# Kernel tuning notes

Hardware: AMD Instinct MI355X
Metric: run time of the kernel (lower is better)

## Reference

```python
import jax, jax.numpy as jnp
import numpy as np

N = 100_000   # nodes
E = 1_600_000 # edges per graph
D = 64        # feature width
HA = 32       # attention hidden


def setup_inputs() -> dict:
    key = jax.random.key(0)
    ks = jax.random.split(key, 20)
    inp = {}
    inp["h"] = jax.random.normal(ks[0], (N, D), jnp.float32)
    inp["e_od"] = jax.random.normal(ks[1], (E, D), jnp.float32)
    inp["e_ad"] = jax.random.normal(ks[2], (E, D), jnp.float32)
    inp["src_od"] = jax.random.randint(ks[3], (E,), 0, N)
    inp["dst_od"] = jax.random.randint(ks[4], (E,), 0, N)
    inp["src_ad"] = jax.random.randint(ks[5], (E,), 0, N)
    inp["dst_ad"] = jax.random.randint(ks[6], (E,), 0, N)
    s = 1.0 / np.sqrt(D).astype(np.float32)
    # stacked params: index 0 = OD graph, index 1 = AD graph
    inp["W_src"]  = jax.random.normal(ks[7],  (2, D, D), jnp.float32) * s
    inp["W_dst"]  = jax.random.normal(ks[8],  (2, D, D), jnp.float32) * s
    inp["W_edge"] = jax.random.normal(ks[9],  (2, D, D), jnp.float32) * s
    inp["b_msg"]  = jnp.zeros((2, D), jnp.float32)
    inp["W_self"] = jax.random.normal(ks[10], (2, D, D), jnp.float32) * s
    inp["W_agg"]  = jax.random.normal(ks[11], (2, D, D), jnp.float32) * s
    inp["b_node"] = jnp.zeros((2, D), jnp.float32)
    # Attention (Aggregate_samedim): Linear(D->HA, bias) -> tanh -> Linear(HA->1, no bias)
    inp["attn_l1_w"] = jax.random.normal(ks[12], (D, HA), jnp.float32) * s
    inp["attn_l1_b"] = jnp.zeros((HA,), jnp.float32)
    inp["attn_l2_w"] = jax.random.normal(ks[13], (HA, 1), jnp.float32) * (1.0 / np.sqrt(HA).astype(np.float32))
    return inp


def reference(h, e_od, e_ad, src_od, dst_od, src_ad, dst_ad,
              W_src, W_dst, W_edge, b_msg, W_self, W_agg, b_node,
              attn_l1_w, attn_l1_b, attn_l2_w):
    def mpnn(i, e, src, dst):
        # edge message: gather src/dst node feats, small GEMMs, relu  [E, D]
        m = jax.nn.relu(h[src] @ W_src[i] + h[dst] @ W_dst[i] + e @ W_edge[i] + b_msg[i])
        # scatter-sum to destination nodes  [N, D]
        agg = jax.ops.segment_sum(m, dst, num_segments=N)
        # node update  [N, D]
        return jax.nn.relu(h @ W_self[i] + agg @ W_agg[i] + b_node[i])

    intra = mpnn(0, e_od, src_od, dst_od)  # OD graph node states
    inter = mpnn(1, e_ad, src_ad, dst_ad)  # AD graph node states
    # Aggregate_samedim: attention over the 2-way stack
    rep = jnp.stack([intra, inter], axis=1)               # [N, 2, D]
    w = jnp.tanh(rep @ attn_l1_w + attn_l1_b) @ attn_l2_w  # [N, 2, 1]
    beta = jax.nn.softmax(w, axis=1)
    return (beta * rep).sum(axis=1)                        # [N, D]
```

## Files before the change

### kernel.cpp

```cpp
#include <hip/hip_runtime.h>
#include <hip/hip_bf16.h>

using short8  = __attribute__((ext_vector_type(8))) short;
using ushort8 = __attribute__((ext_vector_type(8))) unsigned short;
using f32x4   = __attribute__((ext_vector_type(4))) float;
using fvec4   = __attribute__((ext_vector_type(4))) float;

#define CH 8192

__device__ inline unsigned short f2bf(float x) {
  union { __hip_bfloat16 b; unsigned short u; } c;
  c.b = __float2bfloat16(x);
  return c.u;
}
__device__ inline float bf2f(unsigned short s) {
  return __uint_as_float(((unsigned int)s) << 16);
}
__device__ inline unsigned int pk2(float lo, float hi) {
  union { __hip_bfloat162 b; unsigned int u; } c;
  c.b = __float22bfloat162_rn(make_float2(lo, hi));
  return c.u;
}
__device__ inline short8 cvt8(fvec4 a, fvec4 b) {
  union { short8 s; unsigned int u[4]; } r;
  r.u[0] = pk2(a[0], a[1]);
  r.u[1] = pk2(a[2], a[3]);
  r.u[2] = pk2(b[0], b[1]);
  r.u[3] = pk2(b[2], b[3]);
  return r.s;
}

__device__ inline void load_bfrags_f32(const float* __restrict__ W, short8 bfr[2][4], int lane) {
  int l15 = lane & 15, lh = lane >> 4;
#pragma unroll
  for (int ks = 0; ks < 2; ++ks)
#pragma unroll
    for (int ct = 0; ct < 4; ++ct) {
      short8 v;
#pragma unroll
      for (int i = 0; i < 8; ++i)
        v[i] = (short)f2bf(W[(ks * 32 + lh * 8 + i) * 64 + ct * 16 + l15]);
      bfr[ks][ct] = v;
    }
}

__device__ inline void load_bfrags(const unsigned short* __restrict__ Wf, short8 bfr[2][4], int lane) {
#pragma unroll
  for (int ks = 0; ks < 2; ++ks)
#pragma unroll
    for (int ct = 0; ct < 4; ++ct) {
      union { ushort8 u; short8 s; } c;
      c.u = *reinterpret_cast<const ushort8*>(Wf + (((ks * 4 + ct) << 9) + (lane << 3)));
      bfr[ks][ct] = c.s;
    }
}

struct PrepArgs {
  const float* W[10];
};

__global__ __launch_bounds__(64) void prep_w_kernel(PrepArgs pw, unsigned short* __restrict__ Wf) {
  int z = blockIdx.x;
  int lane = threadIdx.x & 63;
  short8 bfr[2][4];
  load_bfrags_f32(pw.W[z], bfr, lane);
  unsigned short* dst = Wf + (size_t)z * 4096;
#pragma unroll
  for (int ks = 0; ks < 2; ++ks)
#pragma unroll
    for (int ct = 0; ct < 4; ++ct) {
      union { short8 s; ushort8 u; } c;
      c.s = bfr[ks][ct];
      *reinterpret_cast<ushort8*>(dst + (((ks * 4 + ct) << 9) + (lane << 3))) = c.u;
    }
}

struct ProjArgs {
  unsigned short* out[6];
};

__global__ __launch_bounds__(256) void proj_all_kernel(const float* __restrict__ h,
                                                       const unsigned short* __restrict__ Wf,
                                                       ProjArgs pa, int N) {
  int lane = threadIdx.x & 63;
  int wv = threadIdx.x >> 6;
  int rowbase = blockIdx.x * 256 + wv * 64;
  int l15 = lane & 15, lh = lane >> 4;

  short8 afr[4][2];
#pragma unroll
  for (int rt = 0; rt < 4; ++rt) {
    int row = rowbase + rt * 16 + l15;
    int rc = row < N ? row : 0;
    const fvec4* p = reinterpret_cast<const fvec4*>(h + (size_t)rc * 64);
#pragma unroll
    for (int ks = 0; ks < 2; ++ks)
      afr[rt][ks] = cvt8(p[ks * 8 + lh * 2], p[ks * 8 + lh * 2 + 1]);
  }

  for (int z = 0; z < 6; ++z) {
    short8 bfr[2][4];
    load_bfrags(Wf + (size_t)z * 4096, bfr, lane);
    unsigned short* __restrict__ out = pa.out[z];

    f32x4 acc[4][4];
#pragma unroll
    for (int rt = 0; rt < 4; ++rt)
#pragma unroll
      for (int ct = 0; ct < 4; ++ct) acc[rt][ct] = (f32x4){0.f, 0.f, 0.f, 0.f};

#pragma unroll
    for (int rt = 0; rt < 4; ++rt)
#pragma unroll
      for (int ks = 0; ks < 2; ++ks)
#pragma unroll
        for (int ct = 0; ct < 4; ++ct)
          acc[rt][ct] = __builtin_amdgcn_mfma_f32_16x16x32_bf16(afr[rt][ks], bfr[ks][ct], acc[rt][ct], 0, 0, 0);

#pragma unroll
    for (int rt = 0; rt < 4; ++rt)
#pragma unroll
      for (int rg = 0; rg < 4; ++rg) {
        int row = rowbase + rt * 16 + lh * 4 + rg;
        if (row < N) {
#pragma unroll
          for (int ct = 0; ct < 4; ++ct)
            out[(size_t)row * 64 + ct * 16 + l15] = f2bf(acc[rt][ct][rg]);
        }
      }
  }
}

__global__ __launch_bounds__(256) void hist_kernel(const int* __restrict__ dst0, const int* __restrict__ dst1,
                                                   int* __restrict__ counts, int E, int NBK) {
  __shared__ int hcnt[2048];
  int z = blockIdx.y;
  const int* __restrict__ dst = z ? dst1 : dst0;
  int t = threadIdx.x;
  for (int i = t; i < NBK; i += 256) hcnt[i] = 0;
  __syncthreads();
  int base = blockIdx.x * CH;
#pragma unroll 4
  for (int k = 0; k < CH / 256; ++k) {
    int i = base + k * 256 + t;
    if (i < E) atomicAdd(&hcnt[dst[i] >> 6], 1);
  }
  __syncthreads();
  for (int i = t; i < NBK; i += 256) {
    int c = hcnt[i];
    if (c) atomicAdd(&counts[(size_t)z * NBK + i], c);
  }
}

__global__ __launch_bounds__(1024) void scan_kernel(const int* __restrict__ counts, int* __restrict__ cursor,
                                                    int* __restrict__ gcur, int NBK) {
  int z = blockIdx.x;
  const int* c = counts + (size_t)z * NBK;
  __shared__ int lds[1024];
  int t = threadIdx.x;
  int carry = 0;
  for (int base = 0; base < NBK; base += 1024) {
    int i = base + t;
    int v = (i < NBK) ? c[i] : 0;
    lds[t] = v;
    __syncthreads();
    for (int off = 1; off < 1024; off <<= 1) {
      int x = (t >= off) ? lds[t - off] : 0;
      __syncthreads();
      lds[t] += x;
      __syncthreads();
    }
    if (i < NBK) {
      int excl = carry + lds[t] - v;
      cursor[(size_t)z * NBK + i] = excl;
      gcur[(size_t)z * NBK + i] = excl;
    }
    carry += lds[1023];
    __syncthreads();
  }
}

__global__ __launch_bounds__(256) void scatterA_kernel(
    const int* __restrict__ src0, const int* __restrict__ dst0,
    const int* __restrict__ src1, const int* __restrict__ dst1,
    int* __restrict__ gcur, int2* __restrict__ recs0, int2* __restrict__ recs1,
    int E, int NBK) {
  __shared__ int lcnt[2048];
  int z = blockIdx.y;
  const int* __restrict__ src = z ? src1 : src0;
  const int* __restrict__ dst = z ? dst1 : dst0;
  int2* __restrict__ recs = z ? recs1 : recs0;
  int t = threadIdx.x;
  for (int i = t; i < NBK; i += 256) lcnt[i] = 0;
  __syncthreads();
  int base = blockIdx.x * CH;
#pragma unroll 4
  for (int k = 0; k < CH / 256; ++k) {
    int i = base + k * 256 + t;
    if (i < E) atomicAdd(&lcnt[dst[i] >> 6], 1);
  }
  __syncthreads();
  for (int i = t; i < NBK; i += 256) {
    int c = lcnt[i];
    lcnt[i] = c ? atomicAdd(&gcur[(size_t)z * NBK + i], c) : 0;
  }
  __syncthreads();
#pragma unroll 4
  for (int k = 0; k < CH / 256; ++k) {
    int i = base + k * 256 + t;
    if (i < E) {
      int d = dst[i], s = src[i];
      int bin = d >> 6, dl = d & 63;
      int pos = atomicAdd(&lcnt[bin], 1);
      recs[pos] = make_int2(i | (bin << 21), s | (dl << 26));
    }
  }
}

__global__ __launch_bounds__(256) void sortB_kernel(int2* __restrict__ recs0, int2* __restrict__ recs1,
                                                    const int* __restrict__ cursor,
                                                    const int* __restrict__ counts, int NBK) {
  __shared__ int cnt_lds[64];
  __shared__ int cur_lds[64];
  int z = blockIdx.y;
  int b = blockIdx.x;
  int2* __restrict__ recs = z ? recs1 : recs0;
  int start = cursor[(size_t)z * NBK + b];
  int cnt = counts[(size_t)z * NBK + b];
  int t = threadIdx.x;

  for (int cbase = 0; cbase < cnt; cbase += 2048) {
    int ccnt = min(2048, cnt - cbase);
    int2 r[8];
    int dl[8];
    if (t < 64) cnt_lds[t] = 0;
    __syncthreads();
#pragma unroll
    for (int k = 0; k < 8; ++k) {
      int idx = k * 256 + t;
      if (idx < ccnt) {
        r[k] = recs[start + cbase + idx];
        dl[k] = ((unsigned)r[k].y) >> 26;
        atomicAdd(&cnt_lds[dl[k]], 1);
      }
    }
    __syncthreads();
    if (t < 64) {
      int c = cnt_lds[t];
      int x = c;
#pragma unroll
      for (int off = 1; off < 64; off <<= 1) {
        int y = __shfl_up(x, off);
        if (t >= off) x += y;
      }
      cur_lds[t] = x - c;
    }
    __syncthreads();
#pragma unroll
    for (int k = 0; k < 8; ++k) {
      int idx = k * 256 + t;
      if (idx < ccnt) {
        int pos = atomicAdd(&cur_lds[dl[k]], 1);
        recs[start + cbase + pos] = r[k];
      }
    }
    __syncthreads();
  }
}

struct EdgeArgs {
  const float* e[2];
  const int2* recs[2];
  const unsigned short* We[2];
  const float* bmsg[2];
  const unsigned short* Ps[2];
  const unsigned short* Pd[2];
  float* agg[2];
};

__global__ __launch_bounds__(256) void edge_sorted_kernel(EdgeArgs ea, int E) {
  int z = blockIdx.y;
  const float* __restrict__ e = ea.e[z];
  const int2* __restrict__ recs = ea.recs[z];
  const unsigned short* __restrict__ Psrc = ea.Ps[z];
  const unsigned short* __restrict__ Pdst = ea.Pd[z];
  float* __restrict__ agg = ea.agg[z];

  int lane = threadIdx.x & 63;
  int wv = threadIdx.x >> 6;
  int base = (blockIdx.x * 4 + wv) * 64;
  if (base >= E) return;
  int l15 = lane & 15, lh = lane >> 4;

  int slot = base + lane;
  int el = 0, sl = 0, dl = 0;
  if (slot < E) {
    int2 rc = recs[slot];
    el = rc.x & 0x1FFFFF;
    sl = rc.y & 0x3FFFFFF;
    dl = (((rc.x >> 21) & 0x7FF) << 6) | (int)(((unsigned)rc.y) >> 26);
  }

  short8 bfr[2][4];
  load_bfrags(ea.We[z], bfr, lane);

  short8 idf[2];
#pragma unroll
  for (int half = 0; half < 2; ++half) {
    short8 v;
#pragma unroll
    for (int i = 0; i < 8; ++i)
      v[i] = (short)((lh * 8 + i == half * 16 + l15) ? 0x3F80 : 0);
    idf[half] = v;
  }

  const float* bmsg = ea.bmsg[z];
  f32x4 acc[4][4];
#pragma unroll
  for (int ct = 0; ct < 4; ++ct) {
    float b = bmsg[ct * 16 + l15];
    f32x4 bb = (f32x4){b, b, b, b};
#pragma unroll
    for (int rt = 0; rt < 4; ++rt) acc[rt][ct] = bb;
  }

#pragma unroll
  for (int rt = 0; rt < 4; ++rt) {
    int sr = rt * 16 + l15;
    int er = __shfl(el, sr);
    int hr = __shfl(sl, sr);
    int dr = __shfl(dl, sr);
    const fvec4* pr = reinterpret_cast<const fvec4*>(e + ((size_t)er << 6));
    const ushort8* ps = reinterpret_cast<const ushort8*>(Psrc + ((size_t)hr << 6));
    const ushort8* pd = reinterpret_cast<const ushort8*>(Pdst + ((size_t)dr << 6));
    short8 aE0 = cvt8(pr[lh * 2], pr[lh * 2 + 1]);
    short8 aE1 = cvt8(pr[8 + lh * 2], pr[8 + lh * 2 + 1]);
    union { ushort8 u; short8 s; } aP0, aP1, aD0, aD1;
    aP0.u = ps[lh];
    aP1.u = ps[4 + lh];
    aD0.u = pd[lh];
    aD1.u = pd[4 + lh];
#pragma unroll
    for (int ct = 0; ct < 4; ++ct) {
      acc[rt][ct] = __builtin_amdgcn_mfma_f32_16x16x32_bf16(aE0, bfr[0][ct], acc[rt][ct], 0, 0, 0);
      acc[rt][ct] = __builtin_amdgcn_mfma_f32_16x16x32_bf16(aE1, bfr[1][ct], acc[rt][ct], 0, 0, 0);
    }
    acc[rt][0] = __builtin_amdgcn_mfma_f32_16x16x32_bf16(aP0.s, idf[0], acc[rt][0], 0, 0, 0);
    acc[rt][1] = __builtin_amdgcn_mfma_f32_16x16x32_bf16(aP0.s, idf[1], acc[rt][1], 0, 0, 0);
    acc[rt][2] = __builtin_amdgcn_mfma_f32_16x16x32_bf16(aP1.s, idf[0], acc[rt][2], 0, 0, 0);
    acc[rt][3] = __builtin_amdgcn_mfma_f32_16x16x32_bf16(aP1.s, idf[1], acc[rt][3], 0, 0, 0);
    acc[rt][0] = __builtin_amdgcn_mfma_f32_16x16x32_bf16(aD0.s, idf[0], acc[rt][0], 0, 0, 0);
    acc[rt][1] = __builtin_amdgcn_mfma_f32_16x16x32_bf16(aD0.s, idf[1], acc[rt][1], 0, 0, 0);
    acc[rt][2] = __builtin_amdgcn_mfma_f32_16x16x32_bf16(aD1.s, idf[0], acc[rt][2], 0, 0, 0);
    acc[rt][3] = __builtin_amdgcn_mfma_f32_16x16x32_bf16(aD1.s, idf[1], acc[rt][3], 0, 0, 0);
  }

#pragma unroll
  for (int rt = 0; rt < 4; ++rt)
#pragma unroll
    for (int ct = 0; ct < 4; ++ct)
#pragma unroll
      for (int rg = 0; rg < 4; ++rg)
        acc[rt][ct][rg] = fmaxf(acc[rt][ct][rg], 0.f);

  int dprev = __shfl_up(dl, 1);
  unsigned long long bnd = __ballot(lane > 0 && dl != dprev);
  int vrows = min(64, E - base);

  int r0 = 0;
  while (r0 < vrows) {
    unsigned long long rest = (r0 < 63) ? (bnd >> (r0 + 1)) : 0ull;
    int r1 = rest ? (r0 + 1 + __builtin_ctzll(rest)) : 64;
    if (r1 > vrows) r1 = vrows;
    int dcur = __shfl(dl, r0);

    float s0 = 0.f, s1 = 0.f, s2 = 0.f, s3 = 0.f;
#pragma unroll
    for (int rt = 0; rt < 4; ++rt) {
      int rs = rt * 16;
      if (r0 <= rs && r1 >= rs + 16) {
#pragma unroll
        for (int rg = 0; rg < 4; ++rg) {
          s0 += acc[rt][0][rg];
          s1 += acc[rt][1][rg];
          s2 += acc[rt][2][rg];
          s3 += acc[rt][3][rg];
        }
      } else if (r0 < rs + 16 && r1 > rs) {
#pragma unroll
        for (int rg = 0; rg < 4; ++rg) {
          int row = rs + lh * 4 + rg;
          bool in = (row >= r0) && (row < r1);
          s0 += in ? acc[rt][0][rg] : 0.f;
          s1 += in ? acc[rt][1][rg] : 0.f;
          s2 += in ? acc[rt][2][rg] : 0.f;
          s3 += in ? acc[rt][3][rg] : 0.f;
        }
      }
    }
    s0 += __shfl_xor(s0, 16); s0 += __shfl_xor(s0, 32);
    s1 += __shfl_xor(s1, 16); s1 += __shfl_xor(s1, 32);
    s2 += __shfl_xor(s2, 16); s2 += __shfl_xor(s2, 32);
    s3 += __shfl_xor(s3, 16); s3 += __shfl_xor(s3, 32);
    float mine = (lh == 0) ? s0 : (lh == 1) ? s1 : (lh == 2) ? s2 : s3;
    atomicAdd(&agg[(size_t)dcur * 64 + lane], mine);
    r0 = r1;
  }
}

struct NodeArgs {
  const float* agg[2];
  const unsigned short* T[2];
  const float* bn[2];
  unsigned short* U[2];
};

__global__ __launch_bounds__(256) void node_kernel(const unsigned short* __restrict__ Wf,
                                                   NodeArgs na, int N) {
  int z = blockIdx.y;
  const float* __restrict__ agg = na.agg[z];
  const unsigned short* __restrict__ T = na.T[z];
  const float* __restrict__ bn = na.bn[z];
  unsigned short* __restrict__ U = na.U[z];
  int lane = threadIdx.x & 63;
  int wv = threadIdx.x >> 6;
  int rowbase = blockIdx.x * 256 + wv * 64;
  int l15 = lane & 15, lh = lane >> 4;

  short8 bfr[2][4];
  load_bfrags(Wf + (size_t)(8 + z) * 4096, bfr, lane);

  f32x4 acc[4][4];
#pragma unroll
  for (int rt = 0; rt < 4; ++rt)
#pragma unroll
    for (int ct = 0; ct < 4; ++ct) acc[rt][ct] = (f32x4){0.f, 0.f, 0.f, 0.f};

#pragma unroll
  for (int rt = 0; rt < 4; ++rt) {
    int row = rowbase + rt * 16 + l15;
    int rc = row < N ? row : 0;
    const fvec4* p = reinterpret_cast<const fvec4*>(agg + (size_t)rc * 64);
#pragma unroll
    for (int ks = 0; ks < 2; ++ks) {
      fvec4 p0 = p[ks * 8 + lh * 2], p1 = p[ks * 8 + lh * 2 + 1];
      short8 ahi = cvt8(p0, p1);
      fvec4 q0, q1;
#pragma unroll
      for (int i = 0; i < 4; ++i) {
        q0[i] = p0[i] - bf2f((unsigned short)ahi[i]);
        q1[i] = p1[i] - bf2f((unsigned short)ahi[i + 4]);
      }
      short8 alo = cvt8(q0, q1);
#pragma unroll
      for (int ct = 0; ct < 4; ++ct) {
        acc[rt][ct] = __builtin_amdgcn_mfma_f32_16x16x32_bf16(ahi, bfr[ks][ct], acc[rt][ct], 0, 0, 0);
        acc[rt][ct] = __builtin_amdgcn_mfma_f32_16x16x32_bf16(alo, bfr[ks][ct], acc[rt][ct], 0, 0, 0);
      }
    }
  }

  float bv[4];
#pragma unroll
  for (int ct = 0; ct < 4; ++ct) bv[ct] = bn[ct * 16 + l15];

#pragma unroll
  for (int rt = 0; rt < 4; ++rt)
#pragma unroll
    for (int rg = 0; rg < 4; ++rg) {
      int row = rowbase + rt * 16 + lh * 4 + rg;
      if (row < N) {
#pragma unroll
        for (int ct = 0; ct < 4; ++ct) {
          int c = ct * 16 + l15;
          float v = acc[rt][ct][rg] + bf2f(T[(size_t)row * 64 + c]) + bv[ct];
          U[(size_t)row * 64 + c] = f2bf(fmaxf(v, 0.0f));
        }
      }
    }
}

__global__ __launch_bounds__(256) void attn_kernel(
    const unsigned short* __restrict__ U0, const unsigned short* __restrict__ U1,
    const float* __restrict__ l1w, const float* __restrict__ l1b, const float* __restrict__ l2w,
    float* __restrict__ out, int N) {
  int t = threadIdx.x;
  int node = blockIdx.x * 64 + (t >> 2);
  int q = t & 3;
  if (node >= N) return;
  size_t b0 = (size_t)node * 64;

  float a0[8], a1[8];
#pragma unroll
  for (int i = 0; i < 8; ++i) { a0[i] = l1b[q * 8 + i]; a1[i] = a0[i]; }

  for (int k = 0; k < 64; ++k) {
    float u0 = bf2f(U0[b0 + k]);
    float u1 = bf2f(U1[b0 + k]);
#pragma unroll
    for (int i = 0; i < 8; ++i) {
      float w = l1w[k * 32 + q * 8 + i];
      a0[i] += u0 * w;
      a1[i] += u1 * w;
    }
  }
  float w0 = 0.f, w1 = 0.f;
#pragma unroll
  for (int i = 0; i < 8; ++i) {
    float l2 = l2w[q * 8 + i];
    w0 += tanhf(a0[i]) * l2;
    w1 += tanhf(a1[i]) * l2;
  }
  w0 += __shfl_xor(w0, 1, 4); w0 += __shfl_xor(w0, 2, 4);
  w1 += __shfl_xor(w1, 1, 4); w1 += __shfl_xor(w1, 2, 4);

  float m = fmaxf(w0, w1);
  float e0 = expf(w0 - m), e1 = expf(w1 - m);
  float inv = 1.0f / (e0 + e1);
  float be0 = e0 * inv, be1 = e1 * inv;

#pragma unroll
  for (int j = 0; j < 16; ++j) {
    int c = q * 16 + j;
    out[b0 + c] = be0 * bf2f(U0[b0 + c]) + be1 * bf2f(U1[b0 + c]);
  }
}

static inline size_t au(size_t x) { return (x + 255) & ~(size_t)255; }

extern "C" void kernel_launch(void* const* d_in, const int* in_sizes, int n_in,
                              void* d_out, int out_size, void* d_ws, size_t ws_size,
                              hipStream_t stream) {
  const float* h      = (const float*)d_in[0];
  const float* e_od   = (const float*)d_in[1];
  const float* e_ad   = (const float*)d_in[2];
  const int* src_od   = (const int*)d_in[3];
  const int* dst_od   = (const int*)d_in[4];
  const int* src_ad   = (const int*)d_in[5];
  const int* dst_ad   = (const int*)d_in[6];
  const float* W_src  = (const float*)d_in[7];
  const float* W_dst  = (const float*)d_in[8];
  const float* W_edge = (const float*)d_in[9];
  const float* b_msg  = (const float*)d_in[10];
  const float* W_self = (const float*)d_in[11];
  const float* W_agg  = (const float*)d_in[12];
  const float* b_node = (const float*)d_in[13];
  const float* l1w    = (const float*)d_in[14];
  const float* l1b    = (const float*)d_in[15];
  const float* l2w    = (const float*)d_in[16];
  float* out = (float*)d_out;

  int N = in_sizes[0] / 64;
  int E = in_sizes[1] / 64;
  int NBK = (N + 63) >> 6;

  char* ws = (char*)d_ws;
  size_t off = 0;
  int* counts = (int*)(ws + off);   off += au((size_t)2 * NBK * sizeof(int));
  float* agg0 = (float*)(ws + off); off += (size_t)N * 64 * sizeof(float);
  float* agg1 = (float*)(ws + off); off += (size_t)N * 64 * sizeof(float);
  size_t zero_bytes = off;
  int* cursor = (int*)(ws + off);   off += au((size_t)2 * NBK * sizeof(int));
  int* gcur   = (int*)(ws + off);   off += au((size_t)2 * NBK * sizeof(int));
  int2* recs0 = (int2*)(ws + off);  off += au((size_t)E * sizeof(int2));
  int2* recs1 = (int2*)(ws + off);  off += au((size_t)E * sizeof(int2));
  unsigned short* Wf = (unsigned short*)(ws + off); off += au((size_t)10 * 4096 * sizeof(unsigned short));
  size_t NP = au((size_t)N * 64 * sizeof(unsigned short));
  unsigned short* Psrc0 = (unsigned short*)(ws + off); off += NP;
  unsigned short* Pdst0 = (unsigned short*)(ws + off); off += NP;
  unsigned short* Psrc1 = (unsigned short*)(ws + off); off += NP;
  unsigned short* Pdst1 = (unsigned short*)(ws + off); off += NP;
  unsigned short* T0    = (unsigned short*)(ws + off); off += NP;
  unsigned short* T1    = (unsigned short*)(ws + off); off += NP;
  unsigned short* U0 = Psrc0;
  unsigned short* U1 = Psrc1;

  hipMemsetAsync(ws, 0, zero_bytes, stream);

  PrepArgs pw;
  pw.W[0] = W_src;         pw.W[1] = W_dst;
  pw.W[2] = W_src + 4096;  pw.W[3] = W_dst + 4096;
  pw.W[4] = W_self;        pw.W[5] = W_self + 4096;
  pw.W[6] = W_edge;        pw.W[7] = W_edge + 4096;
  pw.W[8] = W_agg;         pw.W[9] = W_agg + 4096;
  prep_w_kernel<<<10, 64, 0, stream>>>(pw, Wf);

  int nb = (N + 255) / 256;
  ProjArgs pa;
  pa.out[0] = Psrc0;
  pa.out[1] = Pdst0;
  pa.out[2] = Psrc1;
  pa.out[3] = Pdst1;
  pa.out[4] = T0;
  pa.out[5] = T1;
  proj_all_kernel<<<nb, 256, 0, stream>>>(h, Wf, pa, N);

  int nch = (E + CH - 1) / CH;
  hist_kernel<<<dim3(nch, 2), 256, 0, stream>>>(dst_od, dst_ad, counts, E, NBK);
  scan_kernel<<<2, 1024, 0, stream>>>(counts, cursor, gcur, NBK);
  scatterA_kernel<<<dim3(nch, 2), 256, 0, stream>>>(src_od, dst_od, src_ad, dst_ad, gcur,
                                                    recs0, recs1, E, NBK);
  sortB_kernel<<<dim3(NBK, 2), 256, 0, stream>>>(recs0, recs1, cursor, counts, NBK);

  int tiles = (E + 63) / 64;
  int eb = (tiles + 3) / 4;
  EdgeArgs ea;
  ea.e[0] = e_od;  ea.recs[0] = recs0; ea.We[0] = Wf + 6 * 4096; ea.bmsg[0] = b_msg;
  ea.Ps[0] = Psrc0; ea.Pd[0] = Pdst0; ea.agg[0] = agg0;
  ea.e[1] = e_ad;  ea.recs[1] = recs1; ea.We[1] = Wf + 7 * 4096; ea.bmsg[1] = b_msg + 64;
  ea.Ps[1] = Psrc1; ea.Pd[1] = Pdst1; ea.agg[1] = agg1;
  edge_sorted_kernel<<<dim3(eb, 2), 256, 0, stream>>>(ea, E);

  NodeArgs na;
  na.agg[0] = agg0; na.T[0] = T0; na.bn[0] = b_node;      na.U[0] = U0;
  na.agg[1] = agg1; na.T[1] = T1; na.bn[1] = b_node + 64; na.U[1] = U1;
  node_kernel<<<dim3(nb, 2), 256, 0, stream>>>(Wf, na, N);

  attn_kernel<<<(N + 63) / 64, 256, 0, stream>>>(U0, U1, l1w, l1b, l2w, out, N);
}
```

Baseline: 587.8 us.

## Stage edge gathers through LDS with direct global-to-LDS loads, smaller edge tiles

The edge kernel now handles 16 edges per wave instead of 64. It gathers edge features and projected src/dst rows straight into swizzled LDS with global_load_lds, then reads MFMA fragments from LDS. The goal is to raise memory-level parallelism and occupancy on the gather-bound edge stage, at the cost of four times as many waves and more redundant weight-fragment loads per edge. The projection kernel is also split across a 3-wide grid so each block computes 2 of the 6 projections, trading repeated reads of h for more parallel blocks.

```diff
diff --git a/kernel.cpp b/kernel.cpp
--- a/kernel.cpp
+++ b/kernel.cpp
@@ -30,6 +30,12 @@
   return r.s;
 }
 
+__device__ inline void gload_lds16(const void* g, void* l) {
+  __builtin_amdgcn_global_load_lds(
+      (const __attribute__((address_space(1))) void*)g,
+      (__attribute__((address_space(3))) void*)l, 16, 0, 0);
+}
+
 __device__ inline void load_bfrags_f32(const float* __restrict__ W, short8 bfr[2][4], int lane) {
   int l15 = lane & 15, lh = lane >> 4;
 #pragma unroll
@@ -82,6 +88,7 @@
 __global__ __launch_bounds__(256) void proj_all_kernel(const float* __restrict__ h,
                                                        const unsigned short* __restrict__ Wf,
                                                        ProjArgs pa, int N) {
+  int zb = blockIdx.y * 2;
   int lane = threadIdx.x & 63;
   int wv = threadIdx.x >> 6;
   int rowbase = blockIdx.x * 256 + wv * 64;
@@ -98,7 +105,8 @@
       afr[rt][ks] = cvt8(p[ks * 8 + lh * 2], p[ks * 8 + lh * 2 + 1]);
   }
 
-  for (int z = 0; z < 6; ++z) {
+  for (int zi = 0; zi < 2; ++zi) {
+    int z = zb + zi;
     short8 bfr[2][4];
     load_bfrags(Wf + (size_t)z * 4096, bfr, lane);
     unsigned short* __restrict__ out = pa.out[z];
@@ -279,6 +287,8 @@
 };
 
 __global__ __launch_bounds__(256) void edge_sorted_kernel(EdgeArgs ea, int E) {
+  __shared__ char lds_all[4][8192];
+
   int z = blockIdx.y;
   const float* __restrict__ e = ea.e[z];
   const int2* __restrict__ recs = ea.recs[z];
@@ -288,11 +298,12 @@
 
   int lane = threadIdx.x & 63;
   int wv = threadIdx.x >> 6;
-  int base = (blockIdx.x * 4 + wv) * 64;
+  int base = (blockIdx.x * 4 + wv) * 16;
   if (base >= E) return;
   int l15 = lane & 15, lh = lane >> 4;
-
-  int slot = base + lane;
+  char* lb = &lds_all[wv][0];
+
+  int slot = base + l15;
   int el = 0, sl = 0, dl = 0;
   if (slot < E) {
     int2 rc = recs[slot];
@@ -301,6 +312,34 @@
     dl = (((rc.x >> 21) & 0x7FF) << 6) | (int)(((unsigned)rc.y) >> 26);
   }
 
+#pragma unroll
+  for (int i = 0; i < 4; ++i) {
+    int r = i * 4 + (lane >> 4);
+    int er = __shfl(el, r);
+    int c = (lane & 15) ^ (r & 7);
+    gload_lds16(e + ((size_t)er << 6) + c * 4, lb + i * 1024);
+  }
+#pragma unroll
+  for (int i = 0; i < 2; ++i) {
+    int r = i * 8 + (lane >> 3);
+    int hr = __shfl(sl, r);
+    int c = (lane & 7) ^ (r & 7);
+    gload_lds16(Psrc + ((size_t)hr << 6) + c * 8, lb + 4096 + i * 1024);
+  }
+#pragma unroll
+  for (int i = 0; i < 2; ++i) {
+    int r = i * 8 + (lane >> 3);
+    int dr = __shfl(dl, r);
+    int c = (lane & 7) ^ (r & 7);
+    gload_lds16(Pdst + ((size_t)dr << 6) + c * 8, lb + 6144 + i * 1024);
+  }
+  __builtin_amdgcn_sched_barrier(0);
+
+  const float* bmsg = ea.bmsg[z];
+  float bv[4];
+#pragma unroll
+  for (int ct = 0; ct < 4; ++ct) bv[ct] = bmsg[ct * 16 + l15];
+
   short8 bfr[2][4];
   load_bfrags(ea.We[z], bfr, lane);
 
@@ -314,88 +353,81 @@
     idf[half] = v;
   }
 
-  const float* bmsg = ea.bmsg[z];
-  f32x4 acc[4][4];
-#pragma unroll
-  for (int ct = 0; ct < 4; ++ct) {
-    float b = bmsg[ct * 16 + l15];
-    f32x4 bb = (f32x4){b, b, b, b};
-#pragma unroll
-    for (int rt = 0; rt < 4; ++rt) acc[rt][ct] = bb;
-  }
-
-#pragma unroll
-  for (int rt = 0; rt < 4; ++rt) {
-    int sr = rt * 16 + l15;
-    int er = __shfl(el, sr);
-    int hr = __shfl(sl, sr);
-    int dr = __shfl(dl, sr);
-    const fvec4* pr = reinterpret_cast<const fvec4*>(e + ((size_t)er << 6));
-    const ushort8* ps = reinterpret_cast<const ushort8*>(Psrc + ((size_t)hr << 6));
-    const ushort8* pd = reinterpret_cast<const ushort8*>(Pdst + ((size_t)dr << 6));
-    short8 aE0 = cvt8(pr[lh * 2], pr[lh * 2 + 1]);
-    short8 aE1 = cvt8(pr[8 + lh * 2], pr[8 + lh * 2 + 1]);
-    union { ushort8 u; short8 s; } aP0, aP1, aD0, aD1;
-    aP0.u = ps[lh];
-    aP1.u = ps[4 + lh];
-    aD0.u = pd[lh];
-    aD1.u = pd[4 + lh];
+  f32x4 acc[4];
+#pragma unroll
+  for (int ct = 0; ct < 4; ++ct)
+    acc[ct] = (f32x4){bv[ct], bv[ct], bv[ct], bv[ct]};
+
+  asm volatile("s_waitcnt vmcnt(0)" ::: "memory");
+  __builtin_amdgcn_sched_barrier(0);
+
+  int r = l15;
+  int xs = r & 7;
+
+  union { ushort8 u; short8 s; } aP0, aP1, aD0, aD1;
+  aP0.u = *reinterpret_cast<ushort8*>(lb + 4096 + (r << 7) + (((lh) ^ xs) << 4));
+  aP1.u = *reinterpret_cast<ushort8*>(lb + 4096 + (r << 7) + (((4 + lh) ^ xs) << 4));
+  aD0.u = *reinterpret_cast<ushort8*>(lb + 6144 + (r << 7) + (((lh) ^ xs) << 4));
+  aD1.u = *reinterpret_cast<ushort8*>(lb + 6144 + (r << 7) + (((4 + lh) ^ xs) << 4));
+  acc[0] = __builtin_amdgcn_mfma_f32_16x16x32_bf16(aP0.s, idf[0], acc[0], 0, 0, 0);
+  acc[1] = __builtin_amdgcn_mfma_f32_16x16x32_bf16(aP0.s, idf[1], acc[1], 0, 0, 0);
+  acc[2] = __builtin_amdgcn_mfma_f32_16x16x32_bf16(aP1.s, idf[0], acc[2], 0, 0, 0);
+  acc[3] = __builtin_amdgcn_mfma_f32_16x16x32_bf16(aP1.s, idf[1], acc[3], 0, 0, 0);
+  acc[0] = __builtin_amdgcn_mfma_f32_16x16x32_bf16(aD0.s, idf[0], acc[0], 0, 0, 0);
+  acc[1] = __builtin_amdgcn_mfma_f32_16x16x32_bf16(aD0.s, idf[1], acc[1], 0, 0, 0);
+  acc[2] = __builtin_amdgcn_mfma_f32_16x16x32_bf16(aD1.s, idf[0], acc[2], 0, 0, 0);
+  acc[3] = __builtin_amdgcn_mfma_f32_16x16x32_bf16(aD1.s, idf[1], acc[3], 0, 0, 0);
+
+  {
+    int rb = r << 8;
+    fvec4 p0 = *reinterpret_cast<const fvec4*>(lb + rb + (((lh * 2) ^ xs) << 4));
+    fvec4 p1 = *reinterpret_cast<const fvec4*>(lb + rb + (((lh * 2 + 1) ^ xs) << 4));
+    fvec4 p2 = *reinterpret_cast<const fvec4*>(lb + rb + (((8 + lh * 2) ^ xs) << 4));
+    fvec4 p3 = *reinterpret_cast<const fvec4*>(lb + rb + (((9 + lh * 2) ^ xs) << 4));
+    short8 aE0 = cvt8(p0, p1);
+    short8 aE1 = cvt8(p2, p3);
 #pragma unroll
     for (int ct = 0; ct < 4; ++ct) {
-      acc[rt][ct] = __builtin_amdgcn_mfma_f32_16x16x32_bf16(aE0, bfr[0][ct], acc[rt][ct], 0, 0, 0);
-      acc[rt][ct] = __builtin_amdgcn_mfma_f32_16x16x32_bf16(aE1, bfr[1][ct], acc[rt][ct], 0, 0, 0);
-    }
-    acc[rt][0] = __builtin_amdgcn_mfma_f32_16x16x32_bf16(aP0.s, idf[0], acc[rt][0], 0, 0, 0);
-    acc[rt][1] = __builtin_amdgcn_mfma_f32_16x16x32_bf16(aP0.s, idf[1], acc[rt][1], 0, 0, 0);
-    acc[rt][2] = __builtin_amdgcn_mfma_f32_16x16x32_bf16(aP1.s, idf[0], acc[rt][2], 0, 0, 0);
-    acc[rt][3] = __builtin_amdgcn_mfma_f32_16x16x32_bf16(aP1.s, idf[1], acc[rt][3], 0, 0, 0);
-    acc[rt][0] = __builtin_amdgcn_mfma_f32_16x16x32_bf16(aD0.s, idf[0], acc[rt][0], 0, 0, 0);
-    acc[rt][1] = __builtin_amdgcn_mfma_f32_16x16x32_bf16(aD0.s, idf[1], acc[rt][1], 0, 0, 0);
-    acc[rt][2] = __builtin_amdgcn_mfma_f32_16x16x32_bf16(aD1.s, idf[0], acc[rt][2], 0, 0, 0);
-    acc[rt][3] = __builtin_amdgcn_mfma_f32_16x16x32_bf16(aD1.s, idf[1], acc[rt][3], 0, 0, 0);
-  }
-
-#pragma unroll
-  for (int rt = 0; rt < 4; ++rt)
-#pragma unroll
-    for (int ct = 0; ct < 4; ++ct)
-#pragma unroll
-      for (int rg = 0; rg < 4; ++rg)
-        acc[rt][ct][rg] = fmaxf(acc[rt][ct][rg], 0.f);
+      acc[ct] = __builtin_amdgcn_mfma_f32_16x16x32_bf16(aE0, bfr[0][ct], acc[ct], 0, 0, 0);
+      acc[ct] = __builtin_amdgcn_mfma_f32_16x16x32_bf16(aE1, bfr[1][ct], acc[ct], 0, 0, 0);
+    }
+  }
+
+#pragma unroll
+  for (int ct = 0; ct < 4; ++ct)
+#pragma unroll
+    for (int rg = 0; rg < 4; ++rg)
+      acc[ct][rg] = fmaxf(acc[ct][rg], 0.f);
 
   int dprev = __shfl_up(dl, 1);
-  unsigned long long bnd = __ballot(lane > 0 && dl != dprev);
-  int vrows = min(64, E - base);
+  unsigned long long bnd = __ballot(lane > 0 && dl != dprev) & 0xFFFFull;
+  int vrows = min(16, E - base);
 
   int r0 = 0;
   while (r0 < vrows) {
-    unsigned long long rest = (r0 < 63) ? (bnd >> (r0 + 1)) : 0ull;
-    int r1 = rest ? (r0 + 1 + __builtin_ctzll(rest)) : 64;
+    unsigned long long rest = bnd >> (r0 + 1);
+    int r1 = rest ? (r0 + 1 + __builtin_ctzll(rest)) : 16;
     if (r1 > vrows) r1 = vrows;
     int dcur = __shfl(dl, r0);
 
     float s0 = 0.f, s1 = 0.f, s2 = 0.f, s3 = 0.f;
-#pragma unroll
-    for (int rt = 0; rt < 4; ++rt) {
-      int rs = rt * 16;
-      if (r0 <= rs && r1 >= rs + 16) {
-#pragma unroll
-        for (int rg = 0; rg < 4; ++rg) {
-          s0 += acc[rt][0][rg];
-          s1 += acc[rt][1][rg];
-          s2 += acc[rt][2][rg];
-          s3 += acc[rt][3][rg];
-        }
-      } else if (r0 < rs + 16 && r1 > rs) {
-#pragma unroll
-        for (int rg = 0; rg < 4; ++rg) {
-          int row = rs + lh * 4 + rg;
-          bool in = (row >= r0) && (row < r1);
-          s0 += in ? acc[rt][0][rg] : 0.f;
-          s1 += in ? acc[rt][1][rg] : 0.f;
-          s2 += in ? acc[rt][2][rg] : 0.f;
-          s3 += in ? acc[rt][3][rg] : 0.f;
-        }
+    if (r0 == 0 && r1 == 16) {
+#pragma unroll
+      for (int rg = 0; rg < 4; ++rg) {
+        s0 += acc[0][rg];
+        s1 += acc[1][rg];
+        s2 += acc[2][rg];
+        s3 += acc[3][rg];
+      }
+    } else {
+#pragma unroll
+      for (int rg = 0; rg < 4; ++rg) {
+        int row = lh * 4 + rg;
+        bool in = (row >= r0) && (row < r1);
+        s0 += in ? acc[0][rg] : 0.f;
+        s1 += in ? acc[1][rg] : 0.f;
+        s2 += in ? acc[2][rg] : 0.f;
+        s3 += in ? acc[3][rg] : 0.f;
       }
     }
     s0 += __shfl_xor(s0, 16); s0 += __shfl_xor(s0, 32);
@@ -593,7 +625,7 @@
   pa.out[3] = Pdst1;
   pa.out[4] = T0;
   pa.out[5] = T1;
-  proj_all_kernel<<<nb, 256, 0, stream>>>(h, Wf, pa, N);
+  proj_all_kernel<<<dim3(nb, 3), 256, 0, stream>>>(h, Wf, pa, N);
 
   int nch = (E + CH - 1) / CH;
   hist_kernel<<<dim3(nch, 2), 256, 0, stream>>>(dst_od, dst_ad, counts, E, NBK);
@@ -602,7 +634,7 @@
                                                     recs0, recs1, E, NBK);
   sortB_kernel<<<dim3(NBK, 2), 256, 0, stream>>>(recs0, recs1, cursor, counts, NBK);
 
-  int tiles = (E + 63) / 64;
+  int tiles = (E + 15) / 16;
   int eb = (tiles + 3) / 4;
   EdgeArgs ea;
   ea.e[0] = e_od;  ea.recs[0] = recs0; ea.We[0] = Wf + 6 * 4096; ea.bmsg[0] = b_msg;
```

Result: faster. 501.2 us (-14.7%).
